# Performance work log

Measured on AMD Instinct MI355X. Metric: run time of the kernel, lower is better.

The kernel has to match this reference:

```python
import jax, jax.numpy as jnp
import numpy as np

NUM_HEADS = 16


def setup_inputs() -> dict:
    key = jax.random.key(0)
    k1, k2, k3, k4 = jax.random.split(key, 4)
    B, N, C = 4, 2048, 1024
    x = jax.random.normal(k1, (B, N, C), dtype=jnp.float32)
    # xavier-uniform-ish scaling for stable softmax
    Wqkv = jax.random.normal(k2, (C, 3 * C), dtype=jnp.float32) * (2.0 / (C + 3 * C)) ** 0.5
    Wproj = jax.random.normal(k3, (C, C), dtype=jnp.float32) * (1.0 / C) ** 0.5
    bproj = jnp.zeros((C,), dtype=jnp.float32)
    mask = jax.random.randint(k4, (B, N), 0, 2, dtype=jnp.int32)  # >0 means masked
    return {"x": x, "Wqkv": Wqkv, "Wproj": Wproj, "bproj": bproj, "mask": mask}


def reference(x, Wqkv, Wproj, bproj, mask):
    B, N, C = x.shape
    H = NUM_HEADS
    Dh = C // H
    scale = Dh ** -0.5
    qkv = x @ Wqkv                                   # [B, N, 3C]
    qkv = qkv.reshape(B, N, 3, H, Dh).transpose(2, 0, 3, 1, 4)  # [3, B, H, N, Dh]
    q, k, v = qkv[0], qkv[1], qkv[2]
    att = jnp.einsum('bhqd,bhkd->bhqk', q, k) * scale  # [B, H, N, N]
    att = jnp.where(mask[:, None, None, :] > 0, jnp.float32(-10000000.0), att)
    att = jax.nn.softmax(att, axis=-1)
    out = jnp.einsum('bhqk,bhkd->bhqd', att, v)      # [B, H, N, Dh]
    out = out.transpose(0, 2, 1, 3).reshape(B, N, C)
    return out @ Wproj + bproj
```

## Files before the change

### kernel.cpp

```cpp
#include <hip/hip_runtime.h>
#include <hip/hip_bf16.h>
#include <cstdint>

typedef __bf16 bf16x8 __attribute__((ext_vector_type(8)));
typedef float f32x4 __attribute__((ext_vector_type(4)));
typedef uint4 __attribute__((may_alias)) uint4a;

typedef __attribute__((address_space(3))) unsigned int   lds_u32;
typedef __attribute__((address_space(1))) const unsigned int gbl_u32;

#define BATCH 4
#define SEQ   2048
#define CDIM  1024
#define NH    16
#define HD    64
#define MROWS (BATCH*SEQ)

#define C1SCALE 0.18033688011112042f

__device__ __forceinline__ unsigned short f2bf(float f) {
    uint32_t u = __builtin_bit_cast(uint32_t, f);
    u += 0x7fffu + ((u >> 16) & 1u);
    return (unsigned short)(u >> 16);
}

#if __has_builtin(__builtin_amdgcn_cvt_pk_bf16_f32)
typedef __bf16 bf16x2 __attribute__((ext_vector_type(2)));
__device__ __forceinline__ uint32_t pk2bf(float a, float b) {
    bf16x2 v = __builtin_amdgcn_cvt_pk_bf16_f32(a, b);
    return __builtin_bit_cast(uint32_t, v);
}
#else
__device__ __forceinline__ uint32_t pk2bf(float a, float b) {
    return (uint32_t)f2bf(a) | ((uint32_t)f2bf(b) << 16);
}
#endif

__device__ __forceinline__ void g2l16(const unsigned short* g, unsigned short* l) {
    __builtin_amdgcn_global_load_lds((gbl_u32*)g, (lds_u32*)l, 16, 0, 0);
}

#define NB_CVT   8192
#define NB_TQKV  3072
#define NB_TPROJ 1024
#define NB_PREP  (NB_CVT + NB_TQKV + NB_TPROJ + 4)

__global__ __launch_bounds__(256)
void prep_kernel(const float* __restrict__ x,
                 const float* __restrict__ Wqkv,
                 const float* __restrict__ Wproj,
                 const int* __restrict__ mask,
                 unsigned short* __restrict__ xb,
                 unsigned short* __restrict__ Wqkvt,
                 unsigned short* __restrict__ Wprojt,
                 int* __restrict__ pfx, int* __restrict__ cnt) {
    __shared__ float tile[32][33];
    __shared__ int s[256];
    int bid = blockIdx.x, tid = threadIdx.x;

    if (bid < NB_CVT) {
        int i = (bid * 256 + tid) * 4;
        float4 v = *(const float4*)(x + i);
        uint2 o;
        o.x = pk2bf(v.x, v.y);
        o.y = pk2bf(v.z, v.w);
        *(uint2*)(xb + i) = o;
        return;
    }
    if (bid < NB_CVT + NB_TQKV + NB_TPROJ) {
        const float* in;
        unsigned short* out;
        int Cc, bx;
        if (bid < NB_CVT + NB_TQKV) {
            bx = bid - NB_CVT; in = Wqkv; out = Wqkvt; Cc = 3072;
        } else {
            bx = bid - NB_CVT - NB_TQKV; in = Wproj; out = Wprojt; Cc = 1024;
        }
        int nbx = Cc >> 5;
        int c0 = (bx % nbx) * 32, r0 = (bx / nbx) * 32;
        int tx = tid & 31, ty = tid >> 5;
        #pragma unroll
        for (int i = 0; i < 32; i += 8)
            tile[ty + i][tx] = in[(size_t)(r0 + ty + i) * Cc + c0 + tx];
        __syncthreads();
        #pragma unroll
        for (int i = 0; i < 32; i += 8)
            out[(size_t)(c0 + ty + i) * 1024 + r0 + tx] = f2bf(tile[tx][ty + i]);
        return;
    }
    int b = bid - (NB_CVT + NB_TQKV + NB_TPROJ);
    int keep[8], lc = 0;
    #pragma unroll
    for (int u = 0; u < 8; ++u) {
        keep[u] = (mask[b * SEQ + tid * 8 + u] > 0) ? 0 : 1;
        lc += keep[u];
    }
    s[tid] = lc;
    __syncthreads();
    for (int d = 1; d < 256; d <<= 1) {
        int w = (tid >= d) ? s[tid - d] : 0;
        __syncthreads();
        s[tid] += w;
        __syncthreads();
    }
    int pos = s[tid] - lc;
    #pragma unroll
    for (int u = 0; u < 8; ++u) {
        int idx = b * SEQ + tid * 8 + u;
        pfx[idx] = keep[u] ? pos++ : -1;
    }
    if (tid == 255) cnt[b] = s[255];
}

#define BK 64

__global__ __launch_bounds__(256, 2)
void gemm_qkv_kernel(const unsigned short* __restrict__ A,
                     const unsigned short* __restrict__ Bt,
                     const int* __restrict__ pfx,
                     unsigned short* __restrict__ Q,
                     unsigned short* __restrict__ Kc,
                     unsigned short* __restrict__ Vct) {
    __shared__ __align__(16) unsigned short sA[128 * 64];
    __shared__ __align__(16) unsigned short sB[128 * 64];
    const int Kdim = 1024;
    int m0 = blockIdx.x * 128;
    int n0 = blockIdx.y * 128;
    int tid = threadIdx.x;
    int wave = tid >> 6, lane = tid & 63;
    int wm = (wave >> 1) * 64, wn = (wave & 1) * 64;
    int l15 = lane & 15, quad = lane >> 4;
    int lr = lane >> 3, lc8 = ((lane & 7) ^ lr) * 8;

    f32x4 acc[4][4] = {};

    for (int k0 = 0; k0 < Kdim; k0 += BK) {
        #pragma unroll
        for (int it = 0; it < 4; ++it) {
            int c = wave * 4 + it;
            int gr = c * 8 + lr;
            g2l16(A  + (size_t)(m0 + gr) * Kdim + k0 + lc8, &sA[c * 512]);
            g2l16(Bt + (size_t)(n0 + gr) * Kdim + k0 + lc8, &sB[c * 512]);
        }
        __syncthreads();
        #pragma unroll
        for (int kk = 0; kk < BK; kk += 32) {
            bf16x8 af[4], bfr[4];
            #pragma unroll
            for (int i = 0; i < 4; ++i) {
                int r = wm + i * 16 + l15;
                int q = ((kk >> 3) + quad) ^ (r & 7);
                af[i] = __builtin_bit_cast(bf16x8, *(const uint4a*)(&sA[r * 64 + q * 8]));
            }
            #pragma unroll
            for (int j = 0; j < 4; ++j) {
                int r = wn + j * 16 + l15;
                int q = ((kk >> 3) + quad) ^ (r & 7);
                bfr[j] = __builtin_bit_cast(bf16x8, *(const uint4a*)(&sB[r * 64 + q * 8]));
            }
            #pragma unroll
            for (int i = 0; i < 4; ++i)
                #pragma unroll
                for (int j = 0; j < 4; ++j)
                    acc[i][j] = __builtin_amdgcn_mfma_f32_16x16x32_bf16(af[i], bfr[j], acc[i][j], 0, 0, 0);
        }
        __syncthreads();
    }

    #pragma unroll
    for (int i = 0; i < 4; ++i) {
        #pragma unroll
        for (int j = 0; j < 4; ++j) {
            int col = n0 + wn + j * 16 + l15;
            int three = col >> 10;
            int h = (col >> 6) & 15;
            int d = col & 63;
            int row0 = m0 + wm + i * 16 + quad * 4;
            int b = row0 >> 11, n = row0 & 2047;
            size_t bh = (size_t)(b * NH + h);
            if (three == 0) {
                uint32_t p01 = pk2bf(acc[i][j][0] * C1SCALE, acc[i][j][1] * C1SCALE);
                uint32_t p23 = pk2bf(acc[i][j][2] * C1SCALE, acc[i][j][3] * C1SCALE);
                size_t base = (bh * SEQ + n) * HD + d;
                Q[base]          = (unsigned short)p01;
                Q[base + HD]     = (unsigned short)(p01 >> 16);
                Q[base + 2 * HD] = (unsigned short)p23;
                Q[base + 3 * HD] = (unsigned short)(p23 >> 16);
            } else if (three == 1) {
                #pragma unroll
                for (int r = 0; r < 4; ++r) {
                    int pf = pfx[(b << 11) + n + r];
                    if (pf >= 0) Kc[(bh * SEQ + pf) * HD + d] = f2bf(acc[i][j][r]);
                }
            } else {
                #pragma unroll
                for (int r = 0; r < 4; ++r) {
                    int pf = pfx[(b << 11) + n + r];
                    if (pf >= 0) Vct[(bh * HD + d) * SEQ + pf] = f2bf(acc[i][j][r]);
                }
            }
        }
    }
}

__global__ __launch_bounds__(256, 2)
void gemm_proj_kernel(const unsigned short* __restrict__ A,
                      const unsigned short* __restrict__ Bt,
                      const float* __restrict__ bias,
                      float* __restrict__ Out) {
    __shared__ __align__(16) unsigned short sA[128 * 64];
    __shared__ __align__(16) unsigned short sB[128 * 64];
    const int Kdim = 1024;
    int m0 = blockIdx.x * 128;
    int n0 = blockIdx.y * 128;
    int tid = threadIdx.x;
    int wave = tid >> 6, lane = tid & 63;
    int wm = (wave >> 1) * 64, wn = (wave & 1) * 64;
    int l15 = lane & 15, quad = lane >> 4;
    int lr = lane >> 3, lc8 = ((lane & 7) ^ lr) * 8;

    f32x4 acc[4][4] = {};

    for (int k0 = 0; k0 < Kdim; k0 += BK) {
        #pragma unroll
        for (int it = 0; it < 4; ++it) {
            int c = wave * 4 + it;
            int gr = c * 8 + lr;
            g2l16(A  + (size_t)(m0 + gr) * Kdim + k0 + lc8, &sA[c * 512]);
            g2l16(Bt + (size_t)(n0 + gr) * Kdim + k0 + lc8, &sB[c * 512]);
        }
        __syncthreads();
        #pragma unroll
        for (int kk = 0; kk < BK; kk += 32) {
            bf16x8 af[4], bfr[4];
            #pragma unroll
            for (int i = 0; i < 4; ++i) {
                int r = wm + i * 16 + l15;
                int q = ((kk >> 3) + quad) ^ (r & 7);
                af[i] = __builtin_bit_cast(bf16x8, *(const uint4a*)(&sA[r * 64 + q * 8]));
            }
            #pragma unroll
            for (int j = 0; j < 4; ++j) {
                int r = wn + j * 16 + l15;
                int q = ((kk >> 3) + quad) ^ (r & 7);
                bfr[j] = __builtin_bit_cast(bf16x8, *(const uint4a*)(&sB[r * 64 + q * 8]));
            }
            #pragma unroll
            for (int i = 0; i < 4; ++i)
                #pragma unroll
                for (int j = 0; j < 4; ++j)
                    acc[i][j] = __builtin_amdgcn_mfma_f32_16x16x32_bf16(af[i], bfr[j], acc[i][j], 0, 0, 0);
        }
        __syncthreads();
    }

    #pragma unroll
    for (int i = 0; i < 4; ++i) {
        #pragma unroll
        for (int j = 0; j < 4; ++j) {
            int col = n0 + wn + j * 16 + l15;
            float bv = bias[col];
            #pragma unroll
            for (int r = 0; r < 4; ++r) {
                int row = m0 + wm + i * 16 + quad * 4 + r;
                Out[(size_t)row * CDIM + col] = acc[i][j][r] + bv;
            }
        }
    }
}

#define SPD 72

__global__ __launch_bounds__(256, 4)
void flash_attn_kernel(const unsigned short* __restrict__ Q,
                       const unsigned short* __restrict__ Kg,
                       const unsigned short* __restrict__ Vt,
                       const int* __restrict__ cnt,
                       unsigned short* __restrict__ O) {
    int bh = blockIdx.x;
    int q0 = blockIdx.y * 128;
    int b = bh >> 4, h = bh & 15;
    int tid = threadIdx.x;
    int wave = tid >> 6, lane = tid & 63;
    int l15 = lane & 15, quad = lane >> 4;
    int lr = lane >> 3, lc8 = ((lane & 7) ^ lr) * 8;

    const int kn = cnt[b];

    const size_t head_off = (size_t)bh * SEQ * HD;
    const unsigned short* Qh = Q + head_off;
    const unsigned short* Kh = Kg + head_off;
    const unsigned short* Vh = Vt + head_off;

    __shared__ __align__(16) unsigned short sK [64 * 64];
    __shared__ __align__(16) unsigned short sVt[64 * 64];
    __shared__ __align__(16) unsigned short sP [4][16 * SPD];

    bf16x8 qf[2][2];
    #pragma unroll
    for (int mt = 0; mt < 2; ++mt) {
        const unsigned short* qp = Qh + (size_t)(q0 + wave * 32 + mt * 16 + l15) * HD + quad * 8;
        qf[mt][0] = __builtin_bit_cast(bf16x8, *(const uint4a*)(qp));
        qf[mt][1] = __builtin_bit_cast(bf16x8, *(const uint4a*)(qp + 32));
    }

    bf16x8 ones;
    {
        uint4 ov;
        ov.x = ov.y = ov.z = ov.w = 0x3F803F80u;
        ones = __builtin_bit_cast(bf16x8, ov);
    }

    f32x4 oacc[2][4] = {};
    f32x4 oextra[2] = {};

    for (int k0 = 0; k0 < kn; k0 += 64) {
        #pragma unroll
        for (int it = 0; it < 2; ++it) {
            int c = wave * 2 + it;
            int gr = c * 8 + lr;
            g2l16(Kh + (size_t)(k0 + gr) * HD + lc8, &sK[c * 512]);
            g2l16(Vh + (size_t)gr * SEQ + k0 + lc8, &sVt[c * 512]);
        }
        __syncthreads();

        bool tail = (k0 + 64 > kn);

        #pragma unroll
        for (int mt = 0; mt < 2; ++mt) {
            f32x4 s[4] = {};
            #pragma unroll
            for (int j = 0; j < 4; ++j) {
                int r = j * 16 + l15, sw = r & 7;
                uint4 v0 = *(const uint4a*)(&sK[r * 64 + ((quad ^ sw) * 8)]);
                uint4 v1 = *(const uint4a*)(&sK[r * 64 + (((4 + quad) ^ sw) * 8)]);
                s[j] = __builtin_amdgcn_mfma_f32_16x16x32_bf16(qf[mt][0], __builtin_bit_cast(bf16x8, v0), s[j], 0, 0, 0);
                s[j] = __builtin_amdgcn_mfma_f32_16x16x32_bf16(qf[mt][1], __builtin_bit_cast(bf16x8, v1), s[j], 0, 0, 0);
            }
            unsigned short* sp = &sP[wave][0];
            if (tail) {
                #pragma unroll
                for (int j = 0; j < 4; ++j) {
                    float madd = (k0 + j * 16 + l15 < kn) ? 0.f : -1e30f;
                    #pragma unroll
                    for (int r = 0; r < 4; ++r)
                        s[j][r] = __builtin_amdgcn_exp2f(s[j][r] + madd);
                }
            } else {
                #pragma unroll
                for (int j = 0; j < 4; ++j)
                    #pragma unroll
                    for (int r = 0; r < 4; ++r)
                        s[j][r] = __builtin_amdgcn_exp2f(s[j][r]);
            }
            #pragma unroll
            for (int j = 0; j < 4; ++j) {
                uint32_t p01 = pk2bf(s[j][0], s[j][1]);
                uint32_t p23 = pk2bf(s[j][2], s[j][3]);
                int base = quad * 4 * SPD + j * 16 + l15;
                sp[base]           = (unsigned short)p01;
                sp[base + SPD]     = (unsigned short)(p01 >> 16);
                sp[base + 2 * SPD] = (unsigned short)p23;
                sp[base + 3 * SPD] = (unsigned short)(p23 >> 16);
            }
            #pragma unroll
            for (int kc = 0; kc < 2; ++kc) {
                uint4 av = *(const uint4a*)(&sp[l15 * SPD + kc * 32 + quad * 8]);
                bf16x8 af = __builtin_bit_cast(bf16x8, av);
                #pragma unroll
                for (int jd = 0; jd < 4; ++jd) {
                    int r = jd * 16 + l15;
                    int q = ((kc * 4 + quad) ^ (r & 7)) * 8;
                    uint4 bv = *(const uint4a*)(&sVt[r * 64 + q]);
                    oacc[mt][jd] = __builtin_amdgcn_mfma_f32_16x16x32_bf16(af, __builtin_bit_cast(bf16x8, bv), oacc[mt][jd], 0, 0, 0);
                }
                oextra[mt] = __builtin_amdgcn_mfma_f32_16x16x32_bf16(af, ones, oextra[mt], 0, 0, 0);
            }
        }
        __syncthreads();
    }

    #pragma unroll
    for (int mt = 0; mt < 2; ++mt) {
        float rl[4];
        #pragma unroll
        for (int r = 0; r < 4; ++r) rl[r] = __builtin_amdgcn_rcpf(oextra[mt][r]);
        #pragma unroll
        for (int jd = 0; jd < 4; ++jd) {
            int d = jd * 16 + l15;
            size_t base = ((size_t)(b * SEQ + q0 + wave * 32 + mt * 16 + quad * 4)) * CDIM + h * HD + d;
            uint32_t p01 = pk2bf(oacc[mt][jd][0] * rl[0], oacc[mt][jd][1] * rl[1]);
            uint32_t p23 = pk2bf(oacc[mt][jd][2] * rl[2], oacc[mt][jd][3] * rl[3]);
            O[base]            = (unsigned short)p01;
            O[base + CDIM]     = (unsigned short)(p01 >> 16);
            O[base + 2 * CDIM] = (unsigned short)p23;
            O[base + 3 * CDIM] = (unsigned short)(p23 >> 16);
        }
    }
}

extern "C" void kernel_launch(void* const* d_in, const int* in_sizes, int n_in,
                              void* d_out, int out_size, void* d_ws, size_t ws_size,
                              hipStream_t stream) {
    const float* x     = (const float*)d_in[0];
    const float* Wqkv  = (const float*)d_in[1];
    const float* Wproj = (const float*)d_in[2];
    const float* bproj = (const float*)d_in[3];
    const int*   mask  = (const int*)d_in[4];
    float* out = (float*)d_out;

    char* ws = (char*)d_ws;
    unsigned short* xb     = (unsigned short*)(ws);
    unsigned short* Wqkvt  = (unsigned short*)(ws + (16u << 20));
    unsigned short* Wprojt = (unsigned short*)(ws + (22u << 20));
    unsigned short* Qb     = (unsigned short*)(ws + (24u << 20));
    unsigned short* Kb     = (unsigned short*)(ws + (40u << 20));
    unsigned short* Vtb    = (unsigned short*)(ws + (56u << 20));
    int*            pfx    = (int*)(ws + (72u << 20));
    int*            cntb   = (int*)(ws + (72u << 20) + (32u << 10));

    prep_kernel<<<dim3(NB_PREP), dim3(256), 0, stream>>>(x, Wqkv, Wproj, mask,
                                                         xb, Wqkvt, Wprojt, pfx, cntb);
    gemm_qkv_kernel<<<dim3(64, 24), dim3(256), 0, stream>>>(xb, Wqkvt, pfx, Qb, Kb, Vtb);
    flash_attn_kernel<<<dim3(64, 16), dim3(256), 0, stream>>>(Qb, Kb, Vtb, cntb, xb);
    gemm_proj_kernel<<<dim3(64, 8), dim3(256), 0, stream>>>(xb, Wprojt, bproj, out);
}
```

Before: 253.1 us.

## Triple-buffer GEMMs with 256x128 tiles, block swizzle, and MFMA priority hints

Both projection GEMMs move to a shared 256x128 core. It uses a three-slot LDS ring with K-step 32, prefetches two tiles ahead via global_load_lds, and waits with explicit vmcnt plus raw barriers. Blocks are launched 1-D and remapped so neighbouring blocks share tiles for L2 reuse. s_setprio hints are added around the MFMA sections in both the GEMMs and flash attention. The aim is to overlap global loads with compute and raise arithmetic intensity per block, at the cost of more LDS and registers per block, which may lower occupancy.

New measurement: 287.7 us. 13.7% more time.

```diff
diff --git a/kernel.cpp b/kernel.cpp
--- a/kernel.cpp
+++ b/kernel.cpp
@@ -14,7 +14,6 @@
 #define CDIM  1024
 #define NH    16
 #define HD    64
-#define MROWS (BATCH*SEQ)
 
 #define C1SCALE 0.18033688011112042f
 
@@ -39,6 +38,8 @@
 __device__ __forceinline__ void g2l16(const unsigned short* g, unsigned short* l) {
     __builtin_amdgcn_global_load_lds((gbl_u32*)g, (lds_u32*)l, 16, 0, 0);
 }
+
+#define SWAIT(n) asm volatile("s_waitcnt vmcnt(" #n ")" ::: "memory")
 
 #define NB_CVT   8192
 #define NB_TQKV  3072
@@ -112,7 +113,94 @@
     if (tid == 255) cnt[b] = s[255];
 }
 
-#define BK 64
+#define NTILES  32
+#define SLOT_SH 12288
+#define GEMM_LDS_BYTES (SLOT_SH * 3 * 2)
+
+__device__ __forceinline__ void gemm_core_256x128(
+        const unsigned short* __restrict__ A,
+        const unsigned short* __restrict__ Bt,
+        int m0, int n0, unsigned short* lds, f32x4 (&acc)[8][4]) {
+    const int tid  = threadIdx.x;
+    const int wave = tid >> 6, lane = tid & 63;
+    const int wm = (wave >> 1) * 128, wn = (wave & 1) * 64;
+    const int l15 = lane & 15, quad = lane >> 4;
+    const int srow = lane >> 2;
+    const int scol = (((lane & 3) ^ ((lane >> 3) & 3)) << 3);
+
+    const unsigned short* gA = A  + (size_t)(m0 + wave * 64 + srow) * 1024 + scol;
+    const unsigned short* gB = Bt + (size_t)(n0 + wave * 32 + srow) * 1024 + scol;
+    unsigned short* dA = lds + wave * 2048;
+    unsigned short* dB = lds + 8192 + wave * 1024;
+
+    int offA[8], offB[4];
+    #pragma unroll
+    for (int mi = 0; mi < 8; ++mi) {
+        int r = wm + mi * 16 + l15;
+        offA[mi] = r * 32 + ((quad ^ ((r >> 1) & 3)) << 3);
+    }
+    #pragma unroll
+    for (int nj = 0; nj < 4; ++nj) {
+        int r = wn + nj * 16 + l15;
+        offB[nj] = 8192 + r * 32 + ((quad ^ ((r >> 1) & 3)) << 3);
+    }
+
+    auto stage_tile = [&](int tt, int slot) {
+        unsigned short* da = dA + slot * SLOT_SH;
+        unsigned short* db = dB + slot * SLOT_SH;
+        const unsigned short* ga = gA + tt * 32;
+        const unsigned short* gb = gB + tt * 32;
+        g2l16(ga,             da);
+        g2l16(ga + 16 * 1024, da + 512);
+        g2l16(ga + 32 * 1024, da + 1024);
+        g2l16(ga + 48 * 1024, da + 1536);
+        g2l16(gb,             db);
+        g2l16(gb + 16 * 1024, db + 512);
+    };
+
+    stage_tile(0, 0);
+    stage_tile(1, 1);
+
+    int cur = 0;
+    for (int t = 0; t < NTILES; ++t) {
+        if (t + 2 < NTILES) {
+            int s = cur + 2; if (s >= 3) s -= 3;
+            stage_tile(t + 2, s);
+        }
+        int rem = NTILES - 1 - t;
+        if (rem >= 2)      SWAIT(12);
+        else if (rem == 1) SWAIT(6);
+        else               SWAIT(0);
+        __builtin_amdgcn_sched_barrier(0);
+        __builtin_amdgcn_s_barrier();
+        __builtin_amdgcn_sched_barrier(0);
+        asm volatile("" ::: "memory");
+
+        const unsigned short* sb = lds + cur * SLOT_SH;
+        bf16x8 av[8], bv[4];
+        #pragma unroll
+        for (int nj = 0; nj < 4; ++nj)
+            bv[nj] = __builtin_bit_cast(bf16x8, *(const uint4a*)(sb + offB[nj]));
+        #pragma unroll
+        for (int mi = 0; mi < 8; ++mi)
+            av[mi] = __builtin_bit_cast(bf16x8, *(const uint4a*)(sb + offA[mi]));
+
+        __builtin_amdgcn_s_setprio(1);
+        #pragma unroll
+        for (int mi = 0; mi < 8; ++mi)
+            #pragma unroll
+            for (int nj = 0; nj < 4; ++nj)
+                acc[mi][nj] = __builtin_amdgcn_mfma_f32_16x16x32_bf16(av[mi], bv[nj], acc[mi][nj], 0, 0, 0);
+        __builtin_amdgcn_s_setprio(0);
+
+        asm volatile("" ::: "memory");
+        __builtin_amdgcn_sched_barrier(0);
+        __builtin_amdgcn_s_barrier();
+        __builtin_amdgcn_sched_barrier(0);
+
+        cur = cur + 1; if (cur >= 3) cur = 0;
+    }
+}
 
 __global__ __launch_bounds__(256, 2)
 void gemm_qkv_kernel(const unsigned short* __restrict__ A,
@@ -121,66 +209,34 @@
                      unsigned short* __restrict__ Q,
                      unsigned short* __restrict__ Kc,
                      unsigned short* __restrict__ Vct) {
-    __shared__ __align__(16) unsigned short sA[128 * 64];
-    __shared__ __align__(16) unsigned short sB[128 * 64];
-    const int Kdim = 1024;
-    int m0 = blockIdx.x * 128;
-    int n0 = blockIdx.y * 128;
+    extern __shared__ unsigned short lds[];
+    int lin = blockIdx.x;
+    int swz = (lin & 7) * 96 + (lin >> 3);
+    int m0 = (swz & 31) * 256;
+    int n0 = (swz >> 5) * 128;
+
+    f32x4 acc[8][4] = {};
+    gemm_core_256x128(A, Bt, m0, n0, lds, acc);
+
     int tid = threadIdx.x;
     int wave = tid >> 6, lane = tid & 63;
-    int wm = (wave >> 1) * 64, wn = (wave & 1) * 64;
+    int wm = (wave >> 1) * 128, wn = (wave & 1) * 64;
     int l15 = lane & 15, quad = lane >> 4;
-    int lr = lane >> 3, lc8 = ((lane & 7) ^ lr) * 8;
-
-    f32x4 acc[4][4] = {};
-
-    for (int k0 = 0; k0 < Kdim; k0 += BK) {
-        #pragma unroll
-        for (int it = 0; it < 4; ++it) {
-            int c = wave * 4 + it;
-            int gr = c * 8 + lr;
-            g2l16(A  + (size_t)(m0 + gr) * Kdim + k0 + lc8, &sA[c * 512]);
-            g2l16(Bt + (size_t)(n0 + gr) * Kdim + k0 + lc8, &sB[c * 512]);
-        }
-        __syncthreads();
-        #pragma unroll
-        for (int kk = 0; kk < BK; kk += 32) {
-            bf16x8 af[4], bfr[4];
-            #pragma unroll
-            for (int i = 0; i < 4; ++i) {
-                int r = wm + i * 16 + l15;
-                int q = ((kk >> 3) + quad) ^ (r & 7);
-                af[i] = __builtin_bit_cast(bf16x8, *(const uint4a*)(&sA[r * 64 + q * 8]));
-            }
-            #pragma unroll
-            for (int j = 0; j < 4; ++j) {
-                int r = wn + j * 16 + l15;
-                int q = ((kk >> 3) + quad) ^ (r & 7);
-                bfr[j] = __builtin_bit_cast(bf16x8, *(const uint4a*)(&sB[r * 64 + q * 8]));
-            }
-            #pragma unroll
-            for (int i = 0; i < 4; ++i)
-                #pragma unroll
-                for (int j = 0; j < 4; ++j)
-                    acc[i][j] = __builtin_amdgcn_mfma_f32_16x16x32_bf16(af[i], bfr[j], acc[i][j], 0, 0, 0);
-        }
-        __syncthreads();
-    }
-
-    #pragma unroll
-    for (int i = 0; i < 4; ++i) {
-        #pragma unroll
-        for (int j = 0; j < 4; ++j) {
-            int col = n0 + wn + j * 16 + l15;
+
+    #pragma unroll
+    for (int mi = 0; mi < 8; ++mi) {
+        #pragma unroll
+        for (int nj = 0; nj < 4; ++nj) {
+            int col = n0 + wn + nj * 16 + l15;
             int three = col >> 10;
             int h = (col >> 6) & 15;
             int d = col & 63;
-            int row0 = m0 + wm + i * 16 + quad * 4;
+            int row0 = m0 + wm + mi * 16 + quad * 4;
             int b = row0 >> 11, n = row0 & 2047;
             size_t bh = (size_t)(b * NH + h);
             if (three == 0) {
-                uint32_t p01 = pk2bf(acc[i][j][0] * C1SCALE, acc[i][j][1] * C1SCALE);
-                uint32_t p23 = pk2bf(acc[i][j][2] * C1SCALE, acc[i][j][3] * C1SCALE);
+                uint32_t p01 = pk2bf(acc[mi][nj][0] * C1SCALE, acc[mi][nj][1] * C1SCALE);
+                uint32_t p23 = pk2bf(acc[mi][nj][2] * C1SCALE, acc[mi][nj][3] * C1SCALE);
                 size_t base = (bh * SEQ + n) * HD + d;
                 Q[base]          = (unsigned short)p01;
                 Q[base + HD]     = (unsigned short)(p01 >> 16);
@@ -190,13 +246,13 @@
                 #pragma unroll
                 for (int r = 0; r < 4; ++r) {
                     int pf = pfx[(b << 11) + n + r];
-                    if (pf >= 0) Kc[(bh * SEQ + pf) * HD + d] = f2bf(acc[i][j][r]);
+                    if (pf >= 0) Kc[(bh * SEQ + pf) * HD + d] = f2bf(acc[mi][nj][r]);
                 }
             } else {
                 #pragma unroll
                 for (int r = 0; r < 4; ++r) {
                     int pf = pfx[(b << 11) + n + r];
-                    if (pf >= 0) Vct[(bh * HD + d) * SEQ + pf] = f2bf(acc[i][j][r]);
+                    if (pf >= 0) Vct[(bh * HD + d) * SEQ + pf] = f2bf(acc[mi][nj][r]);
                 }
             }
         }
@@ -208,62 +264,30 @@
                       const unsigned short* __restrict__ Bt,
                       const float* __restrict__ bias,
                       float* __restrict__ Out) {
-    __shared__ __align__(16) unsigned short sA[128 * 64];
-    __shared__ __align__(16) unsigned short sB[128 * 64];
-    const int Kdim = 1024;
-    int m0 = blockIdx.x * 128;
-    int n0 = blockIdx.y * 128;
+    extern __shared__ unsigned short lds[];
+    int lin = blockIdx.x;
+    int swz = (lin & 7) * 32 + (lin >> 3);
+    int m0 = (swz & 31) * 256;
+    int n0 = (swz >> 5) * 128;
+
+    f32x4 acc[8][4] = {};
+    gemm_core_256x128(A, Bt, m0, n0, lds, acc);
+
     int tid = threadIdx.x;
     int wave = tid >> 6, lane = tid & 63;
-    int wm = (wave >> 1) * 64, wn = (wave & 1) * 64;
+    int wm = (wave >> 1) * 128, wn = (wave & 1) * 64;
     int l15 = lane & 15, quad = lane >> 4;
-    int lr = lane >> 3, lc8 = ((lane & 7) ^ lr) * 8;
-
-    f32x4 acc[4][4] = {};
-
-    for (int k0 = 0; k0 < Kdim; k0 += BK) {
-        #pragma unroll
-        for (int it = 0; it < 4; ++it) {
-            int c = wave * 4 + it;
-            int gr = c * 8 + lr;
-            g2l16(A  + (size_t)(m0 + gr) * Kdim + k0 + lc8, &sA[c * 512]);
-            g2l16(Bt + (size_t)(n0 + gr) * Kdim + k0 + lc8, &sB[c * 512]);
-        }
-        __syncthreads();
-        #pragma unroll
-        for (int kk = 0; kk < BK; kk += 32) {
-            bf16x8 af[4], bfr[4];
-            #pragma unroll
-            for (int i = 0; i < 4; ++i) {
-                int r = wm + i * 16 + l15;
-                int q = ((kk >> 3) + quad) ^ (r & 7);
-                af[i] = __builtin_bit_cast(bf16x8, *(const uint4a*)(&sA[r * 64 + q * 8]));
-            }
-            #pragma unroll
-            for (int j = 0; j < 4; ++j) {
-                int r = wn + j * 16 + l15;
-                int q = ((kk >> 3) + quad) ^ (r & 7);
-                bfr[j] = __builtin_bit_cast(bf16x8, *(const uint4a*)(&sB[r * 64 + q * 8]));
-            }
-            #pragma unroll
-            for (int i = 0; i < 4; ++i)
-                #pragma unroll
-                for (int j = 0; j < 4; ++j)
-                    acc[i][j] = __builtin_amdgcn_mfma_f32_16x16x32_bf16(af[i], bfr[j], acc[i][j], 0, 0, 0);
-        }
-        __syncthreads();
-    }
-
-    #pragma unroll
-    for (int i = 0; i < 4; ++i) {
-        #pragma unroll
-        for (int j = 0; j < 4; ++j) {
-            int col = n0 + wn + j * 16 + l15;
+
+    #pragma unroll
+    for (int mi = 0; mi < 8; ++mi) {
+        #pragma unroll
+        for (int nj = 0; nj < 4; ++nj) {
+            int col = n0 + wn + nj * 16 + l15;
             float bv = bias[col];
             #pragma unroll
             for (int r = 0; r < 4; ++r) {
-                int row = m0 + wm + i * 16 + quad * 4 + r;
-                Out[(size_t)row * CDIM + col] = acc[i][j][r] + bv;
+                int row = m0 + wm + mi * 16 + quad * 4 + r;
+                Out[(size_t)row * CDIM + col] = acc[mi][nj][r] + bv;
             }
         }
     }
@@ -334,8 +358,10 @@
                 int r = j * 16 + l15, sw = r & 7;
                 uint4 v0 = *(const uint4a*)(&sK[r * 64 + ((quad ^ sw) * 8)]);
                 uint4 v1 = *(const uint4a*)(&sK[r * 64 + (((4 + quad) ^ sw) * 8)]);
+                __builtin_amdgcn_s_setprio(1);
                 s[j] = __builtin_amdgcn_mfma_f32_16x16x32_bf16(qf[mt][0], __builtin_bit_cast(bf16x8, v0), s[j], 0, 0, 0);
                 s[j] = __builtin_amdgcn_mfma_f32_16x16x32_bf16(qf[mt][1], __builtin_bit_cast(bf16x8, v1), s[j], 0, 0, 0);
+                __builtin_amdgcn_s_setprio(0);
             }
             unsigned short* sp = &sP[wave][0];
             if (tail) {
@@ -367,6 +393,7 @@
             for (int kc = 0; kc < 2; ++kc) {
                 uint4 av = *(const uint4a*)(&sp[l15 * SPD + kc * 32 + quad * 8]);
                 bf16x8 af = __builtin_bit_cast(bf16x8, av);
+                __builtin_amdgcn_s_setprio(1);
                 #pragma unroll
                 for (int jd = 0; jd < 4; ++jd) {
                     int r = jd * 16 + l15;
@@ -375,6 +402,7 @@
                     oacc[mt][jd] = __builtin_amdgcn_mfma_f32_16x16x32_bf16(af, __builtin_bit_cast(bf16x8, bv), oacc[mt][jd], 0, 0, 0);
                 }
                 oextra[mt] = __builtin_amdgcn_mfma_f32_16x16x32_bf16(af, ones, oextra[mt], 0, 0, 0);
+                __builtin_amdgcn_s_setprio(0);
             }
         }
         __syncthreads();
@@ -419,9 +447,18 @@
     int*            pfx    = (int*)(ws + (72u << 20));
     int*            cntb   = (int*)(ws + (72u << 20) + (32u << 10));
 
+    static bool attr_set = false;
+    if (!attr_set) {
+        (void)hipFuncSetAttribute(reinterpret_cast<const void*>(gemm_qkv_kernel),
+                                  hipFuncAttributeMaxDynamicSharedMemorySize, GEMM_LDS_BYTES);
+        (void)hipFuncSetAttribute(reinterpret_cast<const void*>(gemm_proj_kernel),
+                                  hipFuncAttributeMaxDynamicSharedMemorySize, GEMM_LDS_BYTES);
+        attr_set = true;
+    }
+
     prep_kernel<<<dim3(NB_PREP), dim3(256), 0, stream>>>(x, Wqkv, Wproj, mask,
                                                          xb, Wqkvt, Wprojt, pfx, cntb);
-    gemm_qkv_kernel<<<dim3(64, 24), dim3(256), 0, stream>>>(xb, Wqkvt, pfx, Qb, Kb, Vtb);
+    gemm_qkv_kernel<<<dim3(768), dim3(256), GEMM_LDS_BYTES, stream>>>(xb, Wqkvt, pfx, Qb, Kb, Vtb);
     flash_attn_kernel<<<dim3(64, 16), dim3(256), 0, stream>>>(Qb, Kb, Vtb, cntb, xb);
-    gemm_proj_kernel<<<dim3(64, 8), dim3(256), 0, stream>>>(xb, Wprojt, bproj, out);
-}
+    gemm_proj_kernel<<<dim3(256), dim3(256), GEMM_LDS_BYTES, stream>>>(xb, Wprojt, bproj, out);
+}
```

## Load K and V fragments directly from global memory, dropping shared staging

Applied to the files above, without the earlier changes.

The attention kernel no longer stages K and V^T tiles through shared memory with block-wide barriers. Each wave now loads its MFMA operand fragments straight from global memory (through the caches) into registers. s_setprio hints are placed around the MFMA groups. This removes the LDS round trip and the two __syncthreads per key block, but every wave now reads the full K/V tiles redundantly from global/L2 with less coalesced access, and global-load latency is exposed inside the loop.

Result: slower. 371.2 us (+46.6%).

```diff
diff --git a/kernel.cpp b/kernel.cpp
--- a/kernel.cpp
+++ b/kernel.cpp
@@ -283,7 +283,6 @@
     int tid = threadIdx.x;
     int wave = tid >> 6, lane = tid & 63;
     int l15 = lane & 15, quad = lane >> 4;
-    int lr = lane >> 3, lc8 = ((lane & 7) ^ lr) * 8;
 
     const int kn = cnt[b];
 
@@ -292,9 +291,7 @@
     const unsigned short* Kh = Kg + head_off;
     const unsigned short* Vh = Vt + head_off;
 
-    __shared__ __align__(16) unsigned short sK [64 * 64];
-    __shared__ __align__(16) unsigned short sVt[64 * 64];
-    __shared__ __align__(16) unsigned short sP [4][16 * SPD];
+    __shared__ __align__(16) unsigned short sP[4][16 * SPD];
 
     bf16x8 qf[2][2];
     #pragma unroll
@@ -314,30 +311,31 @@
     f32x4 oacc[2][4] = {};
     f32x4 oextra[2] = {};
 
+    const unsigned short* kp0 = Kh + (size_t)l15 * HD + quad * 8;
+    const unsigned short* vp0 = Vh + (size_t)l15 * SEQ + quad * 8;
+
     for (int k0 = 0; k0 < kn; k0 += 64) {
-        #pragma unroll
-        for (int it = 0; it < 2; ++it) {
-            int c = wave * 2 + it;
-            int gr = c * 8 + lr;
-            g2l16(Kh + (size_t)(k0 + gr) * HD + lc8, &sK[c * 512]);
-            g2l16(Vh + (size_t)gr * SEQ + k0 + lc8, &sVt[c * 512]);
-        }
-        __syncthreads();
-
         bool tail = (k0 + 64 > kn);
+
+        bf16x8 kf[4][2];
+        #pragma unroll
+        for (int j = 0; j < 4; ++j) {
+            const unsigned short* kp = kp0 + (size_t)(k0 + j * 16) * HD;
+            kf[j][0] = __builtin_bit_cast(bf16x8, *(const uint4a*)(kp));
+            kf[j][1] = __builtin_bit_cast(bf16x8, *(const uint4a*)(kp + 32));
+        }
 
         #pragma unroll
         for (int mt = 0; mt < 2; ++mt) {
             f32x4 s[4] = {};
+            __builtin_amdgcn_s_setprio(1);
             #pragma unroll
             for (int j = 0; j < 4; ++j) {
-                int r = j * 16 + l15, sw = r & 7;
-                uint4 v0 = *(const uint4a*)(&sK[r * 64 + ((quad ^ sw) * 8)]);
-                uint4 v1 = *(const uint4a*)(&sK[r * 64 + (((4 + quad) ^ sw) * 8)]);
-                s[j] = __builtin_amdgcn_mfma_f32_16x16x32_bf16(qf[mt][0], __builtin_bit_cast(bf16x8, v0), s[j], 0, 0, 0);
-                s[j] = __builtin_amdgcn_mfma_f32_16x16x32_bf16(qf[mt][1], __builtin_bit_cast(bf16x8, v1), s[j], 0, 0, 0);
-            }
-            unsigned short* sp = &sP[wave][0];
+                s[j] = __builtin_amdgcn_mfma_f32_16x16x32_bf16(qf[mt][0], kf[j][0], s[j], 0, 0, 0);
+                s[j] = __builtin_amdgcn_mfma_f32_16x16x32_bf16(qf[mt][1], kf[j][1], s[j], 0, 0, 0);
+            }
+            __builtin_amdgcn_s_setprio(0);
+
             if (tail) {
                 #pragma unroll
                 for (int j = 0; j < 4; ++j) {
@@ -353,6 +351,7 @@
                     for (int r = 0; r < 4; ++r)
                         s[j][r] = __builtin_amdgcn_exp2f(s[j][r]);
             }
+            unsigned short* sp = &sP[wave][0];
             #pragma unroll
             for (int j = 0; j < 4; ++j) {
                 uint32_t p01 = pk2bf(s[j][0], s[j][1]);
@@ -367,17 +366,16 @@
             for (int kc = 0; kc < 2; ++kc) {
                 uint4 av = *(const uint4a*)(&sp[l15 * SPD + kc * 32 + quad * 8]);
                 bf16x8 af = __builtin_bit_cast(bf16x8, av);
+                __builtin_amdgcn_s_setprio(1);
                 #pragma unroll
                 for (int jd = 0; jd < 4; ++jd) {
-                    int r = jd * 16 + l15;
-                    int q = ((kc * 4 + quad) ^ (r & 7)) * 8;
-                    uint4 bv = *(const uint4a*)(&sVt[r * 64 + q]);
+                    uint4 bv = *(const uint4a*)(vp0 + (size_t)jd * 16 * SEQ + k0 + kc * 32);
                     oacc[mt][jd] = __builtin_amdgcn_mfma_f32_16x16x32_bf16(af, __builtin_bit_cast(bf16x8, bv), oacc[mt][jd], 0, 0, 0);
                 }
                 oextra[mt] = __builtin_amdgcn_mfma_f32_16x16x32_bf16(af, ones, oextra[mt], 0, 0, 0);
-            }
-        }
-        __syncthreads();
+                __builtin_amdgcn_s_setprio(0);
+            }
+        }
     }
 
     #pragma unroll
```

## Split QKV GEMM and compute K/V only for unmasked rows via gather

Applied to the files above, without the earlier changes.

The fused QKV projection is split into a Q GEMM over all rows and a K/V GEMM that gathers only unmasked token rows through a compacted row-index list built in the prep kernel. Blocks past the kept count exit early, so roughly half of the K/V projection work is skipped given the random mask. The attention kernel also raises wave priority around its MFMA sequences with s_setprio. The cost is an extra kernel launch and indirect row addressing in the A loads.

New measurement: 238.8 us. -5.7%, faster.

```diff
diff --git a/kernel.cpp b/kernel.cpp
--- a/kernel.cpp
+++ b/kernel.cpp
@@ -14,7 +14,6 @@
 #define CDIM  1024
 #define NH    16
 #define HD    64
-#define MROWS (BATCH*SEQ)
 
 #define C1SCALE 0.18033688011112042f
 
@@ -53,7 +52,7 @@
                  unsigned short* __restrict__ xb,
                  unsigned short* __restrict__ Wqkvt,
                  unsigned short* __restrict__ Wprojt,
-                 int* __restrict__ pfx, int* __restrict__ cnt) {
+                 int* __restrict__ ridx, int* __restrict__ cnt) {
     __shared__ float tile[32][33];
     __shared__ int s[256];
     int bid = blockIdx.x, tid = threadIdx.x;
@@ -106,21 +105,20 @@
     int pos = s[tid] - lc;
     #pragma unroll
     for (int u = 0; u < 8; ++u) {
-        int idx = b * SEQ + tid * 8 + u;
-        pfx[idx] = keep[u] ? pos++ : -1;
-    }
-    if (tid == 255) cnt[b] = s[255];
+        if (keep[u]) ridx[b * SEQ + pos++] = tid * 8 + u;
+    }
+    int total = s[255];
+    for (int i = total + tid; i < SEQ; i += 256)
+        ridx[b * SEQ + i] = 0;
+    if (tid == 255) cnt[b] = total;
 }
 
 #define BK 64
 
 __global__ __launch_bounds__(256, 2)
-void gemm_qkv_kernel(const unsigned short* __restrict__ A,
-                     const unsigned short* __restrict__ Bt,
-                     const int* __restrict__ pfx,
-                     unsigned short* __restrict__ Q,
-                     unsigned short* __restrict__ Kc,
-                     unsigned short* __restrict__ Vct) {
+void gemm_q_kernel(const unsigned short* __restrict__ A,
+                   const unsigned short* __restrict__ Bt,
+                   unsigned short* __restrict__ Q) {
     __shared__ __align__(16) unsigned short sA[128 * 64];
     __shared__ __align__(16) unsigned short sB[128 * 64];
     const int Kdim = 1024;
@@ -172,31 +170,107 @@
         #pragma unroll
         for (int j = 0; j < 4; ++j) {
             int col = n0 + wn + j * 16 + l15;
-            int three = col >> 10;
-            int h = (col >> 6) & 15;
+            int h = col >> 6;
             int d = col & 63;
             int row0 = m0 + wm + i * 16 + quad * 4;
             int b = row0 >> 11, n = row0 & 2047;
             size_t bh = (size_t)(b * NH + h);
+            uint32_t p01 = pk2bf(acc[i][j][0] * C1SCALE, acc[i][j][1] * C1SCALE);
+            uint32_t p23 = pk2bf(acc[i][j][2] * C1SCALE, acc[i][j][3] * C1SCALE);
+            size_t base = (bh * SEQ + n) * HD + d;
+            Q[base]          = (unsigned short)p01;
+            Q[base + HD]     = (unsigned short)(p01 >> 16);
+            Q[base + 2 * HD] = (unsigned short)p23;
+            Q[base + 3 * HD] = (unsigned short)(p23 >> 16);
+        }
+    }
+}
+
+__global__ __launch_bounds__(256, 2)
+void gemm_kv_kernel(const unsigned short* __restrict__ A,
+                    const unsigned short* __restrict__ Bt,
+                    const int* __restrict__ ridx,
+                    const int* __restrict__ cnt,
+                    unsigned short* __restrict__ Kc,
+                    unsigned short* __restrict__ Vct) {
+    __shared__ __align__(16) unsigned short sA[128 * 64];
+    __shared__ __align__(16) unsigned short sB[128 * 64];
+    const int Kdim = 1024;
+    int b  = blockIdx.x >> 4;
+    int m0 = (blockIdx.x & 15) * 128;
+    const int kn = cnt[b];
+    if (m0 >= kn) return;
+    int n0 = 1024 + blockIdx.y * 128;
+    int tid = threadIdx.x;
+    int wave = tid >> 6, lane = tid & 63;
+    int wm = (wave >> 1) * 64, wn = (wave & 1) * 64;
+    int l15 = lane & 15, quad = lane >> 4;
+    int lr = lane >> 3, lc8 = ((lane & 7) ^ lr) * 8;
+
+    const unsigned short* aRow[4];
+    #pragma unroll
+    for (int it = 0; it < 4; ++it) {
+        int gr = (wave * 4 + it) * 8 + lr;
+        int rid = ridx[b * SEQ + m0 + gr];
+        aRow[it] = A + (size_t)(b * SEQ + rid) * Kdim + lc8;
+    }
+
+    f32x4 acc[4][4] = {};
+
+    for (int k0 = 0; k0 < Kdim; k0 += BK) {
+        #pragma unroll
+        for (int it = 0; it < 4; ++it) {
+            int c = wave * 4 + it;
+            int gr = c * 8 + lr;
+            g2l16(aRow[it] + k0, &sA[c * 512]);
+            g2l16(Bt + (size_t)(n0 + gr) * Kdim + k0 + lc8, &sB[c * 512]);
+        }
+        __syncthreads();
+        #pragma unroll
+        for (int kk = 0; kk < BK; kk += 32) {
+            bf16x8 af[4], bfr[4];
+            #pragma unroll
+            for (int i = 0; i < 4; ++i) {
+                int r = wm + i * 16 + l15;
+                int q = ((kk >> 3) + quad) ^ (r & 7);
+                af[i] = __builtin_bit_cast(bf16x8, *(const uint4a*)(&sA[r * 64 + q * 8]));
+            }
+            #pragma unroll
+            for (int j = 0; j < 4; ++j) {
+                int r = wn + j * 16 + l15;
+                int q = ((kk >> 3) + quad) ^ (r & 7);
+                bfr[j] = __builtin_bit_cast(bf16x8, *(const uint4a*)(&sB[r * 64 + q * 8]));
+            }
+            #pragma unroll
+            for (int i = 0; i < 4; ++i)
+                #pragma unroll
+                for (int j = 0; j < 4; ++j)
+                    acc[i][j] = __builtin_amdgcn_mfma_f32_16x16x32_bf16(af[i], bfr[j], acc[i][j], 0, 0, 0);
+        }
+        __syncthreads();
+    }
+
+    #pragma unroll
+    for (int i = 0; i < 4; ++i) {
+        #pragma unroll
+        for (int j = 0; j < 4; ++j) {
+            int c2 = (n0 - 1024) + wn + j * 16 + l15;
+            int three = c2 >> 10;
+            int h = (c2 >> 6) & 15;
+            int d = c2 & 63;
+            int pf0 = m0 + wm + i * 16 + quad * 4;
+            size_t bh = (size_t)(b * NH + h);
             if (three == 0) {
-                uint32_t p01 = pk2bf(acc[i][j][0] * C1SCALE, acc[i][j][1] * C1SCALE);
-                uint32_t p23 = pk2bf(acc[i][j][2] * C1SCALE, acc[i][j][3] * C1SCALE);
-                size_t base = (bh * SEQ + n) * HD + d;
-                Q[base]          = (unsigned short)p01;
-                Q[base + HD]     = (unsigned short)(p01 >> 16);
-                Q[base + 2 * HD] = (unsigned short)p23;
-                Q[base + 3 * HD] = (unsigned short)(p23 >> 16);
-            } else if (three == 1) {
                 #pragma unroll
                 for (int r = 0; r < 4; ++r) {
-                    int pf = pfx[(b << 11) + n + r];
-                    if (pf >= 0) Kc[(bh * SEQ + pf) * HD + d] = f2bf(acc[i][j][r]);
+                    int pf = pf0 + r;
+                    if (pf < kn) Kc[(bh * SEQ + pf) * HD + d] = f2bf(acc[i][j][r]);
                 }
             } else {
                 #pragma unroll
                 for (int r = 0; r < 4; ++r) {
-                    int pf = pfx[(b << 11) + n + r];
-                    if (pf >= 0) Vct[(bh * HD + d) * SEQ + pf] = f2bf(acc[i][j][r]);
+                    int pf = pf0 + r;
+                    if (pf < kn) Vct[(bh * HD + d) * SEQ + pf] = f2bf(acc[i][j][r]);
                 }
             }
         }
@@ -334,8 +408,10 @@
                 int r = j * 16 + l15, sw = r & 7;
                 uint4 v0 = *(const uint4a*)(&sK[r * 64 + ((quad ^ sw) * 8)]);
                 uint4 v1 = *(const uint4a*)(&sK[r * 64 + (((4 + quad) ^ sw) * 8)]);
+                __builtin_amdgcn_s_setprio(1);
                 s[j] = __builtin_amdgcn_mfma_f32_16x16x32_bf16(qf[mt][0], __builtin_bit_cast(bf16x8, v0), s[j], 0, 0, 0);
                 s[j] = __builtin_amdgcn_mfma_f32_16x16x32_bf16(qf[mt][1], __builtin_bit_cast(bf16x8, v1), s[j], 0, 0, 0);
+                __builtin_amdgcn_s_setprio(0);
             }
             unsigned short* sp = &sP[wave][0];
             if (tail) {
@@ -367,6 +443,7 @@
             for (int kc = 0; kc < 2; ++kc) {
                 uint4 av = *(const uint4a*)(&sp[l15 * SPD + kc * 32 + quad * 8]);
                 bf16x8 af = __builtin_bit_cast(bf16x8, av);
+                __builtin_amdgcn_s_setprio(1);
                 #pragma unroll
                 for (int jd = 0; jd < 4; ++jd) {
                     int r = jd * 16 + l15;
@@ -375,6 +452,7 @@
                     oacc[mt][jd] = __builtin_amdgcn_mfma_f32_16x16x32_bf16(af, __builtin_bit_cast(bf16x8, bv), oacc[mt][jd], 0, 0, 0);
                 }
                 oextra[mt] = __builtin_amdgcn_mfma_f32_16x16x32_bf16(af, ones, oextra[mt], 0, 0, 0);
+                __builtin_amdgcn_s_setprio(0);
             }
         }
         __syncthreads();
@@ -416,12 +494,13 @@
     unsigned short* Qb     = (unsigned short*)(ws + (24u << 20));
     unsigned short* Kb     = (unsigned short*)(ws + (40u << 20));
     unsigned short* Vtb    = (unsigned short*)(ws + (56u << 20));
-    int*            pfx    = (int*)(ws + (72u << 20));
+    int*            ridx   = (int*)(ws + (72u << 20));
     int*            cntb   = (int*)(ws + (72u << 20) + (32u << 10));
 
     prep_kernel<<<dim3(NB_PREP), dim3(256), 0, stream>>>(x, Wqkv, Wproj, mask,
-                                                         xb, Wqkvt, Wprojt, pfx, cntb);
-    gemm_qkv_kernel<<<dim3(64, 24), dim3(256), 0, stream>>>(xb, Wqkvt, pfx, Qb, Kb, Vtb);
+                                                         xb, Wqkvt, Wprojt, ridx, cntb);
+    gemm_q_kernel<<<dim3(64, 8), dim3(256), 0, stream>>>(xb, Wqkvt, Qb);
+    gemm_kv_kernel<<<dim3(64, 16), dim3(256), 0, stream>>>(xb, Wqkvt, ridx, cntb, Kb, Vtb);
     flash_attn_kernel<<<dim3(64, 16), dim3(256), 0, stream>>>(Qb, Kb, Vtb, cntb, xb);
     gemm_proj_kernel<<<dim3(64, 8), dim3(256), 0, stream>>>(xb, Wprojt, bproj, out);
 }
```
